# Optimization experiments

Measured on AMD Instinct MI355X. Metric: run time of the kernel, lower is better.

The kernel has to match this reference:

```python
import jax, jax.numpy as jnp
import numpy as np

DIM = 2048
NUM_HEADS = 16
HEAD_DIM = DIM // NUM_HEADS  # 128


def setup_inputs() -> dict:
    key = jax.random.key(0)
    ks = jax.random.split(key, 5)
    scale = 0.02
    x = jax.random.normal(ks[0], (1, 2048, DIM), dtype=jnp.float32)
    # nn.Linear weights stored as [out_features, in_features]
    Wq = jax.random.normal(ks[1], (DIM, DIM), dtype=jnp.float32) * scale
    Wk = jax.random.normal(ks[2], (HEAD_DIM, DIM), dtype=jnp.float32) * scale
    Wv = jax.random.normal(ks[3], (HEAD_DIM, DIM), dtype=jnp.float32) * scale
    Wo = jax.random.normal(ks[4], (DIM, DIM), dtype=jnp.float32) * scale
    return {"x": x, "Wq": Wq, "Wk": Wk, "Wv": Wv, "Wo": Wo}


def reference(x, Wq, Wk, Wv, Wo):
    batch, seq_len, dim = x.shape
    q = x @ Wq.T                                   # [b, s, dim]
    k = x @ Wk.T                                   # [b, s, head_dim] (shared across heads)
    v = x @ Wv.T                                   # [b, s, head_dim]
    q = q.reshape(batch, seq_len, NUM_HEADS, HEAD_DIM).transpose(0, 2, 1, 3)  # [b, h, s, d]
    # MQA: single KV head broadcast across query heads (no materialized repeat)
    scores = jnp.einsum("bhqd,bkd->bhqk", q, k) / (HEAD_DIM ** 0.5)
    probs = jax.nn.softmax(scores, axis=-1)        # [b, h, q, k]
    out = jnp.einsum("bhqk,bkd->bhqd", probs, v)   # [b, h, s, d]
    out = out.transpose(0, 2, 1, 3).reshape(batch, seq_len, dim)
    return out @ Wo.T
```

## Files before the change

### kernel.cpp

```cpp
#include <hip/hip_runtime.h>

typedef float  float4_t __attribute__((ext_vector_type(4)));
typedef __bf16 bf16x8   __attribute__((ext_vector_type(8)));
typedef unsigned short u16;

__device__ __forceinline__ u16 f2bf(float f) {
    unsigned u = __float_as_uint(f);
    u += 0x7fffu + ((u >> 16) & 1u);
    return (u16)(u >> 16);
}

#define GLOAD_LDS16(g, l)                                              \
    __builtin_amdgcn_global_load_lds(                                  \
        (__attribute__((address_space(1))) void*)(g),                  \
        (__attribute__((address_space(3))) void*)(l), 16, 0, 0)

__global__ __launch_bounds__(256) void cast_all(const float* __restrict__ x,
                                                const float* __restrict__ wq,
                                                const float* __restrict__ wk,
                                                const float* __restrict__ wv,
                                                const float* __restrict__ wo,
                                                u16* __restrict__ xb, u16* __restrict__ wqb,
                                                u16* __restrict__ wkb, u16* __restrict__ wvb,
                                                u16* __restrict__ wob) {
    const int b = blockIdx.x;
    const float* src;
    u16* dst;
    int i;
    if (b < 4096)      { src = x;  dst = xb;  i = b * 256 + threadIdx.x; }
    else if (b < 8192) { src = wq; dst = wqb; i = (b - 4096) * 256 + threadIdx.x; }
    else if (b < 8448) { src = wk; dst = wkb; i = (b - 8192) * 256 + threadIdx.x; }
    else if (b < 8704) { src = wv; dst = wvb; i = (b - 8448) * 256 + threadIdx.x; }
    else               { src = wo; dst = wob; i = (b - 8704) * 256 + threadIdx.x; }
    float4 f = ((const float4*)src)[i];
    ushort4 r;
    r.x = f2bf(f.x); r.y = f2bf(f.y); r.z = f2bf(f.z); r.w = f2bf(f.w);
    ((ushort4*)dst)[i] = r;
}

template <typename EPI>
__device__ __forceinline__ void gemm_core(const u16* __restrict__ A,
                                          const u16* __restrict__ B,
                                          int K, int bm, int bn, EPI epi) {
    __shared__ __align__(16) u16 As[128 * 32];
    __shared__ __align__(16) u16 Bs[128 * 32];
    const int tid  = threadIdx.x;
    const int lane = tid & 63, wave = tid >> 6;
    const int wm = wave >> 1, wn = wave & 1;
    const int quad = lane >> 4, l16 = lane & 15;

    float4_t acc[4][4] = {};
    const int r0 = tid >> 2;
    const int c0 = (tid & 3) * 8;

    for (int k0 = 0; k0 < K; k0 += 32) {
#pragma unroll
        for (int i = 0; i < 2; ++i) {
            const int row = i * 64 + r0;
            const int e   = (i * 256 + tid) * 8;
            GLOAD_LDS16(A + (size_t)(bm + row) * K + k0 + c0, &As[e]);
            GLOAD_LDS16(B + (size_t)(bn + row) * K + k0 + c0, &Bs[e]);
        }
        __syncthreads();

        bf16x8 af[4], bfr[4];
#pragma unroll
        for (int mi = 0; mi < 4; ++mi)
            af[mi] = *(const bf16x8*)&As[(wm * 64 + mi * 16 + l16) * 32 + quad * 8];
#pragma unroll
        for (int ni = 0; ni < 4; ++ni)
            bfr[ni] = *(const bf16x8*)&Bs[(wn * 64 + ni * 16 + l16) * 32 + quad * 8];
#pragma unroll
        for (int mi = 0; mi < 4; ++mi)
#pragma unroll
            for (int ni = 0; ni < 4; ++ni)
                acc[mi][ni] = __builtin_amdgcn_mfma_f32_16x16x32_bf16(
                    af[mi], bfr[ni], acc[mi][ni], 0, 0, 0);
        __syncthreads();
    }

#pragma unroll
    for (int mi = 0; mi < 4; ++mi) {
        const int row = bm + wm * 64 + mi * 16 + quad * 4;
#pragma unroll
        for (int ni = 0; ni < 4; ++ni) {
            const int col = bn + wn * 64 + ni * 16 + l16;
#pragma unroll
            for (int r = 0; r < 4; ++r) epi(row + r, col, acc[mi][ni][r]);
        }
    }
}

__global__ __launch_bounds__(256) void gemm_qkv(const u16* __restrict__ A,
                                                const u16* __restrict__ B,
                                                u16* __restrict__ qb,
                                                u16* __restrict__ kb,
                                                u16* __restrict__ vtb) {
    gemm_core(A, B, 2048, blockIdx.x * 128, blockIdx.y * 128,
              [=](int row, int col, float v) {
                  if (col < 2048)
                      qb[(size_t)row * 2048 + col] = f2bf(v * 0.08838834764831845f);
                  else if (col < 2176)
                      kb[(size_t)row * 128 + (col - 2048)] = f2bf(v);
                  else
                      vtb[(size_t)(col - 2176) * 2048 + row] = f2bf(v);
              });
}

__global__ __launch_bounds__(256) void gemm_out(const u16* __restrict__ A,
                                                const u16* __restrict__ B,
                                                float* __restrict__ C) {
    gemm_core(A, B, 2048, blockIdx.x * 128, blockIdx.y * 128,
              [=](int row, int col, float v) {
                  C[(size_t)row * 2048 + col] = v;
              });
}

__global__ __launch_bounds__(128, 2) void mqa_attn(const u16* __restrict__ Q,
                                                   const u16* __restrict__ Kmat,
                                                   const u16* __restrict__ Vt,
                                                   u16* __restrict__ O) {
    __shared__ __align__(16) u16 Ks[4 * 64 * 32];
    __shared__ __align__(16) u16 Vts[2 * 128 * 32];
    __shared__ __align__(16) u16 Ps[2][32 * 72];
    const int tid  = threadIdx.x;
    const int wave = tid >> 6, lane = tid & 63;
    const int quad = lane >> 4, l16 = lane & 15;
    const int h     = blockIdx.y;
    const int qbase = blockIdx.x * 64 + wave * 32;

    bf16x8 qf[2][4];
#pragma unroll
    for (int mt = 0; mt < 2; ++mt)
#pragma unroll
        for (int kb4 = 0; kb4 < 4; ++kb4)
            qf[mt][kb4] = *(const bf16x8*)(Q + (size_t)(qbase + mt * 16 + l16) * 2048 +
                                           h * 128 + kb4 * 32 + quad * 8);

    float4_t acc[2][8];
#pragma unroll
    for (int mt = 0; mt < 2; ++mt)
#pragma unroll
        for (int nt = 0; nt < 8; ++nt) acc[mt][nt] = (float4_t){0.f, 0.f, 0.f, 0.f};
    float lsum[8] = {};

    u16* pb = Ps[wave];

    for (int s = 0; s < 32; ++s) {
        const int k0 = s * 64;
#pragma unroll
        for (int i = 0; i < 8; ++i) {
            const int slot = i * 128 + tid;
            const int sub = slot >> 8, win = slot & 255;
            const int row = win >> 2, ch = (win & 3) * 8;
            GLOAD_LDS16(Kmat + (size_t)(k0 + row) * 128 + sub * 32 + ch, &Ks[slot * 8]);
        }
#pragma unroll
        for (int i = 0; i < 8; ++i) {
            const int slot = i * 128 + tid;
            const int sub = slot >> 9, win = slot & 511;
            const int row = win >> 2, ch = (win & 3) * 8;
            GLOAD_LDS16(Vt + (size_t)row * 2048 + k0 + sub * 32 + ch, &Vts[slot * 8]);
        }
        __syncthreads();

#pragma unroll
        for (int ct = 0; ct < 4; ++ct) {
            float4_t s0 = (float4_t){0.f, 0.f, 0.f, 0.f};
            float4_t s1 = (float4_t){0.f, 0.f, 0.f, 0.f};
#pragma unroll
            for (int kb4 = 0; kb4 < 4; ++kb4) {
                bf16x8 kf = *(const bf16x8*)&Ks[(kb4 * 64 + ct * 16 + l16) * 32 + quad * 8];
                s0 = __builtin_amdgcn_mfma_f32_16x16x32_bf16(qf[0][kb4], kf, s0, 0, 0, 0);
                s1 = __builtin_amdgcn_mfma_f32_16x16x32_bf16(qf[1][kb4], kf, s1, 0, 0, 0);
            }
#pragma unroll
            for (int r = 0; r < 4; ++r) {
                const float e0 = __expf(s0[r]);
                const float e1 = __expf(s1[r]);
                lsum[r]     += e0;
                lsum[4 + r] += e1;
                pb[(quad * 4 + r) * 72 + ct * 16 + l16]      = f2bf(e0);
                pb[(16 + quad * 4 + r) * 72 + ct * 16 + l16] = f2bf(e1);
            }
        }
        bf16x8 pa[2][2];
#pragma unroll
        for (int mt = 0; mt < 2; ++mt)
#pragma unroll
            for (int kk = 0; kk < 2; ++kk)
                pa[mt][kk] = *(const bf16x8*)&pb[(mt * 16 + l16) * 72 + kk * 32 + quad * 8];
#pragma unroll
        for (int kk = 0; kk < 2; ++kk)
#pragma unroll
            for (int nt = 0; nt < 8; ++nt) {
                bf16x8 vf = *(const bf16x8*)&Vts[(kk * 128 + nt * 16 + l16) * 32 + quad * 8];
                acc[0][nt] = __builtin_amdgcn_mfma_f32_16x16x32_bf16(pa[0][kk], vf, acc[0][nt], 0, 0, 0);
                acc[1][nt] = __builtin_amdgcn_mfma_f32_16x16x32_bf16(pa[1][kk], vf, acc[1][nt], 0, 0, 0);
            }
        __syncthreads();
    }

#pragma unroll
    for (int mt = 0; mt < 2; ++mt)
#pragma unroll
        for (int r = 0; r < 4; ++r) {
            float lrow = lsum[mt * 4 + r];
#pragma unroll
            for (int off = 1; off < 16; off <<= 1) lrow += __shfl_xor(lrow, off);
            const float inv = 1.0f / lrow;
            const size_t rowoff = (size_t)(qbase + mt * 16 + quad * 4 + r) * 2048 + h * 128;
#pragma unroll
            for (int nt = 0; nt < 8; ++nt)
                O[rowoff + nt * 16 + l16] = f2bf(acc[mt][nt][r] * inv);
        }
}

extern "C" void kernel_launch(void* const* d_in, const int* in_sizes, int n_in,
                              void* d_out, int out_size, void* d_ws, size_t ws_size,
                              hipStream_t stream) {
    const float* x  = (const float*)d_in[0];
    const float* Wq = (const float*)d_in[1];
    const float* Wk = (const float*)d_in[2];
    const float* Wv = (const float*)d_in[3];
    const float* Wo = (const float*)d_in[4];
    float* out = (float*)d_out;

    u16* ws   = (u16*)d_ws;
    u16* xb   = ws;
    u16* Wqb  = xb  + (4 << 20);
    u16* Wkb  = Wqb + (4 << 20);
    u16* Wvb  = Wkb + (256 << 10);
    u16* Wob  = Wvb + (256 << 10);
    u16* qb   = Wob + (4 << 20);
    u16* kb   = qb  + (4 << 20);
    u16* vtb  = kb  + (256 << 10);
    u16* attn = vtb + (256 << 10);

    cast_all<<<12800, 256, 0, stream>>>(x, Wq, Wk, Wv, Wo, xb, Wqb, Wkb, Wvb, Wob);

    gemm_qkv<<<dim3(16, 18), 256, 0, stream>>>(xb, Wqb, qb, kb, vtb);
    mqa_attn<<<dim3(32, 16), 128, 0, stream>>>(qb, kb, vtb, attn);
    gemm_out<<<dim3(16, 16), 256, 0, stream>>>(attn, Wob, out);
}
```

Baseline: 260.5 us.

## Split attention over key halves with combine kernel; halve GEMM M-tile

Attention now splits the key range into two halves across blockIdx.z, doubling the grid. Each half writes unnormalized fp32 partial outputs and row sums, and a new combine kernel adds them, normalizes and converts to bf16. Both projection GEMMs switch from 128x128 to 64x128 tiles, doubling their block counts to fill the CUs better. The cost is extra fp32 partial-output traffic, one more kernel launch, and lower per-block reuse in the GEMMs.

```diff
diff --git a/kernel.cpp b/kernel.cpp
--- a/kernel.cpp
+++ b/kernel.cpp
@@ -42,38 +42,37 @@
 __device__ __forceinline__ void gemm_core(const u16* __restrict__ A,
                                           const u16* __restrict__ B,
                                           int K, int bm, int bn, EPI epi) {
-    __shared__ __align__(16) u16 As[128 * 32];
+    __shared__ __align__(16) u16 As[64 * 32];
     __shared__ __align__(16) u16 Bs[128 * 32];
     const int tid  = threadIdx.x;
     const int lane = tid & 63, wave = tid >> 6;
-    const int wm = wave >> 1, wn = wave & 1;
     const int quad = lane >> 4, l16 = lane & 15;
 
-    float4_t acc[4][4] = {};
+    float4_t acc[4][2] = {};
     const int r0 = tid >> 2;
     const int c0 = (tid & 3) * 8;
 
     for (int k0 = 0; k0 < K; k0 += 32) {
+        GLOAD_LDS16(A + (size_t)(bm + r0) * K + k0 + c0, &As[tid * 8]);
 #pragma unroll
         for (int i = 0; i < 2; ++i) {
-            const int row = i * 64 + r0;
-            const int e   = (i * 256 + tid) * 8;
-            GLOAD_LDS16(A + (size_t)(bm + row) * K + k0 + c0, &As[e]);
-            GLOAD_LDS16(B + (size_t)(bn + row) * K + k0 + c0, &Bs[e]);
-        }
-        __syncthreads();
-
-        bf16x8 af[4], bfr[4];
+            const int slot = i * 256 + tid;
+            const int row  = slot >> 2, ch = (slot & 3) * 8;
+            GLOAD_LDS16(B + (size_t)(bn + row) * K + k0 + ch, &Bs[slot * 8]);
+        }
+        __syncthreads();
+
+        bf16x8 af[4], bfr[2];
 #pragma unroll
         for (int mi = 0; mi < 4; ++mi)
-            af[mi] = *(const bf16x8*)&As[(wm * 64 + mi * 16 + l16) * 32 + quad * 8];
-#pragma unroll
-        for (int ni = 0; ni < 4; ++ni)
-            bfr[ni] = *(const bf16x8*)&Bs[(wn * 64 + ni * 16 + l16) * 32 + quad * 8];
+            af[mi] = *(const bf16x8*)&As[(mi * 16 + l16) * 32 + quad * 8];
+#pragma unroll
+        for (int ni = 0; ni < 2; ++ni)
+            bfr[ni] = *(const bf16x8*)&Bs[(wave * 32 + ni * 16 + l16) * 32 + quad * 8];
 #pragma unroll
         for (int mi = 0; mi < 4; ++mi)
 #pragma unroll
-            for (int ni = 0; ni < 4; ++ni)
+            for (int ni = 0; ni < 2; ++ni)
                 acc[mi][ni] = __builtin_amdgcn_mfma_f32_16x16x32_bf16(
                     af[mi], bfr[ni], acc[mi][ni], 0, 0, 0);
         __syncthreads();
@@ -81,10 +80,10 @@
 
 #pragma unroll
     for (int mi = 0; mi < 4; ++mi) {
-        const int row = bm + wm * 64 + mi * 16 + quad * 4;
-#pragma unroll
-        for (int ni = 0; ni < 4; ++ni) {
-            const int col = bn + wn * 64 + ni * 16 + l16;
+        const int row = bm + mi * 16 + quad * 4;
+#pragma unroll
+        for (int ni = 0; ni < 2; ++ni) {
+            const int col = bn + wave * 32 + ni * 16 + l16;
 #pragma unroll
             for (int r = 0; r < 4; ++r) epi(row + r, col, acc[mi][ni][r]);
         }
@@ -96,7 +95,7 @@
                                                 u16* __restrict__ qb,
                                                 u16* __restrict__ kb,
                                                 u16* __restrict__ vtb) {
-    gemm_core(A, B, 2048, blockIdx.x * 128, blockIdx.y * 128,
+    gemm_core(A, B, 2048, blockIdx.x * 64, blockIdx.y * 128,
               [=](int row, int col, float v) {
                   if (col < 2048)
                       qb[(size_t)row * 2048 + col] = f2bf(v * 0.08838834764831845f);
@@ -110,24 +109,28 @@
 __global__ __launch_bounds__(256) void gemm_out(const u16* __restrict__ A,
                                                 const u16* __restrict__ B,
                                                 float* __restrict__ C) {
-    gemm_core(A, B, 2048, blockIdx.x * 128, blockIdx.y * 128,
+    gemm_core(A, B, 2048, blockIdx.x * 64, blockIdx.y * 128,
               [=](int row, int col, float v) {
                   C[(size_t)row * 2048 + col] = v;
               });
 }
 
-__global__ __launch_bounds__(128, 2) void mqa_attn(const u16* __restrict__ Q,
-                                                   const u16* __restrict__ Kmat,
-                                                   const u16* __restrict__ Vt,
-                                                   u16* __restrict__ O) {
-    __shared__ __align__(16) u16 Ks[4 * 64 * 32];
-    __shared__ __align__(16) u16 Vts[2 * 128 * 32];
-    __shared__ __align__(16) u16 Ps[2][32 * 72];
+__global__ __launch_bounds__(128) void mqa_attn(const u16* __restrict__ Q,
+                                                const u16* __restrict__ Kmat,
+                                                const u16* __restrict__ Vt,
+                                                float* __restrict__ Oacc0,
+                                                float* __restrict__ Oacc1,
+                                                float* __restrict__ Lsum) {
+    __shared__ __align__(16) u16 Ks[4 * 32 * 32];
+    __shared__ __align__(16) u16 Vts[128 * 32];
+    __shared__ __align__(16) u16 Ps[2][32 * 40];
     const int tid  = threadIdx.x;
     const int wave = tid >> 6, lane = tid & 63;
     const int quad = lane >> 4, l16 = lane & 15;
     const int h     = blockIdx.y;
+    const int ks    = blockIdx.z;
     const int qbase = blockIdx.x * 64 + wave * 32;
+    const int kbase = ks * 1024;
 
     bf16x8 qf[2][4];
 #pragma unroll
@@ -147,30 +150,29 @@
     u16* pb = Ps[wave];
 
     for (int s = 0; s < 32; ++s) {
-        const int k0 = s * 64;
-#pragma unroll
-        for (int i = 0; i < 8; ++i) {
+        const int k0 = kbase + s * 32;
+#pragma unroll
+        for (int i = 0; i < 4; ++i) {
             const int slot = i * 128 + tid;
-            const int sub = slot >> 8, win = slot & 255;
+            const int kb4 = slot >> 7, win = slot & 127;
             const int row = win >> 2, ch = (win & 3) * 8;
-            GLOAD_LDS16(Kmat + (size_t)(k0 + row) * 128 + sub * 32 + ch, &Ks[slot * 8]);
-        }
-#pragma unroll
-        for (int i = 0; i < 8; ++i) {
+            GLOAD_LDS16(Kmat + (size_t)(k0 + row) * 128 + kb4 * 32 + ch, &Ks[slot * 8]);
+        }
+#pragma unroll
+        for (int i = 0; i < 4; ++i) {
             const int slot = i * 128 + tid;
-            const int sub = slot >> 9, win = slot & 511;
-            const int row = win >> 2, ch = (win & 3) * 8;
-            GLOAD_LDS16(Vt + (size_t)row * 2048 + k0 + sub * 32 + ch, &Vts[slot * 8]);
-        }
-        __syncthreads();
-
-#pragma unroll
-        for (int ct = 0; ct < 4; ++ct) {
+            const int d = slot >> 2, ch = (slot & 3) * 8;
+            GLOAD_LDS16(Vt + (size_t)d * 2048 + k0 + ch, &Vts[slot * 8]);
+        }
+        __syncthreads();
+
+#pragma unroll
+        for (int ct = 0; ct < 2; ++ct) {
             float4_t s0 = (float4_t){0.f, 0.f, 0.f, 0.f};
             float4_t s1 = (float4_t){0.f, 0.f, 0.f, 0.f};
 #pragma unroll
             for (int kb4 = 0; kb4 < 4; ++kb4) {
-                bf16x8 kf = *(const bf16x8*)&Ks[(kb4 * 64 + ct * 16 + l16) * 32 + quad * 8];
+                bf16x8 kf = *(const bf16x8*)&Ks[kb4 * 1024 + (ct * 16 + l16) * 32 + quad * 8];
                 s0 = __builtin_amdgcn_mfma_f32_16x16x32_bf16(qf[0][kb4], kf, s0, 0, 0, 0);
                 s1 = __builtin_amdgcn_mfma_f32_16x16x32_bf16(qf[1][kb4], kf, s1, 0, 0, 0);
             }
@@ -180,40 +182,57 @@
                 const float e1 = __expf(s1[r]);
                 lsum[r]     += e0;
                 lsum[4 + r] += e1;
-                pb[(quad * 4 + r) * 72 + ct * 16 + l16]      = f2bf(e0);
-                pb[(16 + quad * 4 + r) * 72 + ct * 16 + l16] = f2bf(e1);
+                pb[(quad * 4 + r) * 40 + ct * 16 + l16]      = f2bf(e0);
+                pb[(16 + quad * 4 + r) * 40 + ct * 16 + l16] = f2bf(e1);
             }
         }
-        bf16x8 pa[2][2];
+        bf16x8 pa[2];
 #pragma unroll
         for (int mt = 0; mt < 2; ++mt)
-#pragma unroll
-            for (int kk = 0; kk < 2; ++kk)
-                pa[mt][kk] = *(const bf16x8*)&pb[(mt * 16 + l16) * 72 + kk * 32 + quad * 8];
-#pragma unroll
-        for (int kk = 0; kk < 2; ++kk)
-#pragma unroll
-            for (int nt = 0; nt < 8; ++nt) {
-                bf16x8 vf = *(const bf16x8*)&Vts[(kk * 128 + nt * 16 + l16) * 32 + quad * 8];
-                acc[0][nt] = __builtin_amdgcn_mfma_f32_16x16x32_bf16(pa[0][kk], vf, acc[0][nt], 0, 0, 0);
-                acc[1][nt] = __builtin_amdgcn_mfma_f32_16x16x32_bf16(pa[1][kk], vf, acc[1][nt], 0, 0, 0);
-            }
+            pa[mt] = *(const bf16x8*)&pb[(mt * 16 + l16) * 40 + quad * 8];
+#pragma unroll
+        for (int nt = 0; nt < 8; ++nt) {
+            bf16x8 vf = *(const bf16x8*)&Vts[(nt * 16 + l16) * 32 + quad * 8];
+            acc[0][nt] = __builtin_amdgcn_mfma_f32_16x16x32_bf16(pa[0], vf, acc[0][nt], 0, 0, 0);
+            acc[1][nt] = __builtin_amdgcn_mfma_f32_16x16x32_bf16(pa[1], vf, acc[1][nt], 0, 0, 0);
+        }
         __syncthreads();
     }
 
+    float* __restrict__ Op = ks ? Oacc1 : Oacc0;
 #pragma unroll
     for (int mt = 0; mt < 2; ++mt)
 #pragma unroll
         for (int r = 0; r < 4; ++r) {
+            const int row = qbase + mt * 16 + quad * 4 + r;
+            const size_t base = ((size_t)h * 2048 + row) * 128;
             float lrow = lsum[mt * 4 + r];
 #pragma unroll
             for (int off = 1; off < 16; off <<= 1) lrow += __shfl_xor(lrow, off);
-            const float inv = 1.0f / lrow;
-            const size_t rowoff = (size_t)(qbase + mt * 16 + quad * 4 + r) * 2048 + h * 128;
+            if (l16 == 0) Lsum[(size_t)ks * 32768 + h * 2048 + row] = lrow;
 #pragma unroll
             for (int nt = 0; nt < 8; ++nt)
-                O[rowoff + nt * 16 + l16] = f2bf(acc[mt][nt][r] * inv);
-        }
+                Op[base + nt * 16 + l16] = acc[mt][nt][r];
+        }
+}
+
+__global__ __launch_bounds__(256) void attn_combine(const float* __restrict__ O0,
+                                                    const float* __restrict__ O1,
+                                                    const float* __restrict__ L,
+                                                    u16* __restrict__ attn) {
+    const int f = blockIdx.x * 256 + threadIdx.x;
+    const int d4 = f & 31, h = (f >> 5) & 15, q = f >> 9;
+    const int li = h * 2048 + q;
+    const float inv = 1.0f / (L[li] + L[32768 + li]);
+    const int oi = li * 32 + d4;
+    const float4 a = ((const float4*)O0)[oi];
+    const float4 b = ((const float4*)O1)[oi];
+    ushort4 r;
+    r.x = f2bf((a.x + b.x) * inv);
+    r.y = f2bf((a.y + b.y) * inv);
+    r.z = f2bf((a.z + b.z) * inv);
+    r.w = f2bf((a.w + b.w) * inv);
+    ((ushort4*)attn)[f] = r;
 }
 
 extern "C" void kernel_launch(void* const* d_in, const int* in_sizes, int n_in,
@@ -236,10 +255,14 @@
     u16* kb   = qb  + (4 << 20);
     u16* vtb  = kb  + (256 << 10);
     u16* attn = vtb + (256 << 10);
+    float* Oacc0 = (float*)ws;
+    float* Oacc1 = (float*)(attn + (4 << 20));
+    float* Lsum  = Oacc1 + (4 << 20);
 
     cast_all<<<12800, 256, 0, stream>>>(x, Wq, Wk, Wv, Wo, xb, Wqb, Wkb, Wvb, Wob);
 
-    gemm_qkv<<<dim3(16, 18), 256, 0, stream>>>(xb, Wqb, qb, kb, vtb);
-    mqa_attn<<<dim3(32, 16), 128, 0, stream>>>(qb, kb, vtb, attn);
-    gemm_out<<<dim3(16, 16), 256, 0, stream>>>(attn, Wob, out);
-}
+    gemm_qkv<<<dim3(32, 18), 256, 0, stream>>>(xb, Wqb, qb, kb, vtb);
+    mqa_attn<<<dim3(32, 16, 2), 128, 0, stream>>>(qb, kb, vtb, Oacc0, Oacc1, Lsum);
+    attn_combine<<<4096, 256, 0, stream>>>(Oacc0, Oacc1, Lsum, attn);
+    gemm_out<<<dim3(32, 16), 256, 0, stream>>>(attn, Wob, out);
+}
```

New measurement: 240.9 us. 7.5% less time.
